# Kernel tuning notes

Hardware: AMD Instinct MI355X
Metric: run time of the kernel (lower is better)

## Reference

```python
import jax, jax.numpy as jnp
import numpy as np

L2_REG = 0.02


def setup_inputs() -> dict:
    key = jax.random.key(0)
    k1, k2 = jax.random.split(key)
    n, d = 4096, 1024
    anchors = jax.random.normal(k1, (n, d), dtype=jnp.float32)
    positives = jax.random.normal(k2, (n, d), dtype=jnp.float32)
    return {"anchors": anchors, "positives": positives}


def reference(anchors, positives):
    # Fused equivalent of the per-row masked_select loop:
    # x[i, j] = a_i . (p_j - p_i) = S[i, j] - S[i, i], for j != i
    n = anchors.shape[0]
    S = anchors @ positives.T                     # (n, n)
    x = S - jnp.diag(S)[:, None]                  # subtract anchor-positive sim per row
    offdiag = ~jnp.eye(n, dtype=bool)
    # sum over negatives j != i of exp(x[i, j])
    s = jnp.sum(jnp.where(offdiag, jnp.exp(x), 0.0), axis=1)  # (n,)
    n_pair = jnp.mean(jnp.log1p(s))
    l2 = jnp.sum(anchors ** 2 + positives ** 2) / n
    return n_pair + L2_REG * l2
```

## Files before the change

### kernel.cpp

```cpp
#include <hip/hip_runtime.h>
#include <math.h>
#include <stdint.h>

#define N 4096
#define Dm 1024
#define BK 64
#define NT (Dm / BK)
#define NCB (N / 64)
#define NPART 512

typedef __attribute__((ext_vector_type(8))) short bf16x8;
typedef __attribute__((ext_vector_type(4))) float f32x4;

typedef const void __attribute__((address_space(1)))* gas_t;
typedef void __attribute__((address_space(3)))* las_t;

static __device__ __forceinline__ void gload_lds16(const void* g, void* l) {
    __builtin_amdgcn_global_load_lds((gas_t)g, (las_t)l, 16, 0, 0);
}

static __device__ __forceinline__ unsigned short f2bf(float f) {
    unsigned int u = __float_as_uint(f);
    unsigned int r = (u + 0x7fff + ((u >> 16) & 1)) >> 16;
    return (unsigned short)r;
}

__global__ __launch_bounds__(256) void prep_kernel(const float* __restrict__ A,
                                                   const float* __restrict__ P,
                                                   unsigned short* __restrict__ Abf,
                                                   unsigned short* __restrict__ Pbf,
                                                   float* __restrict__ D,
                                                   float* __restrict__ rowl2,
                                                   float* __restrict__ accL,
                                                   float* __restrict__ accR,
                                                   unsigned int* __restrict__ ticket) {
    if (blockIdx.x == 0 && threadIdx.x == 0) {
        accL[0] = 0.0f; accR[0] = 0.0f; ticket[0] = 0u;
    }
    int t = threadIdx.x;
    int lane = t & 63;
    int row = blockIdx.x * 4 + (t >> 6);
    const float4* a4 = (const float4*)(A + (size_t)row * Dm);
    const float4* p4 = (const float4*)(P + (size_t)row * Dm);
    ushort4* ao = (ushort4*)(Abf + (size_t)row * Dm);
    ushort4* po = (ushort4*)(Pbf + (size_t)row * Dm);
    float dot = 0.0f, l2 = 0.0f;
#pragma unroll
    for (int c = 0; c < 4; ++c) {
        int idx = c * 64 + lane;
        float4 a = a4[idx], p = p4[idx];
        ushort4 ab, pb;
        ab.x = f2bf(a.x); ab.y = f2bf(a.y); ab.z = f2bf(a.z); ab.w = f2bf(a.w);
        pb.x = f2bf(p.x); pb.y = f2bf(p.y); pb.z = f2bf(p.z); pb.w = f2bf(p.w);
        ao[idx] = ab; po[idx] = pb;
        dot += a.x * p.x + a.y * p.y + a.z * p.z + a.w * p.w;
        l2  += a.x * a.x + a.y * a.y + a.z * a.z + a.w * a.w
             + p.x * p.x + p.y * p.y + p.z * p.z + p.w * p.w;
    }
#pragma unroll
    for (int off = 32; off; off >>= 1) {
        dot += __shfl_xor(dot, off, 64);
        l2  += __shfl_xor(l2,  off, 64);
    }
    if (lane == 0) {
        D[row]     = dot;
        rowl2[row] = l2;
    }
}

#define STAGE_TILE(gp, lp, kt) do {                                            \
        gload_lds16((gp) + (kt),                    (lp)         + tid * 8);   \
        gload_lds16((gp) + (kt) +  64 * (size_t)Dm, (lp) + 4096  + tid * 8);   \
        gload_lds16((gp) + (kt) + 128 * (size_t)Dm, (lp) + 8192  + tid * 8);   \
        gload_lds16((gp) + (kt) + 192 * (size_t)Dm, (lp) + 12288 + tid * 8);   \
    } while (0)

#define STAGE_B_HALF(lpB, kt, h) do {                                          \
        gload_lds16(gB + (kt) + ((h) ? 128 * (size_t)Dm : (size_t)0),          \
                    (lpB) + (h) * 8192 + tid * 8);                             \
        gload_lds16(gB + (kt) + ((h) ? 192 * (size_t)Dm : 64 * (size_t)Dm),    \
                    (lpB) + (h) * 8192 + 4096 + tid * 8);                      \
    } while (0)

#define READ_A4(dst, buf, rg0) do {                                            \
        dst[0] = *(const bf16x8*)((buf) + ((rg0)     * 16) * BK + aoff0);      \
        dst[1] = *(const bf16x8*)((buf) + ((rg0)     * 16) * BK + aoff1);      \
        dst[2] = *(const bf16x8*)((buf) + ((rg0) + 1) * 16 * BK + aoff0);      \
        dst[3] = *(const bf16x8*)((buf) + ((rg0) + 1) * 16 * BK + aoff1);      \
    } while (0)

#define READ_B8(buf) do {                                                      \
        _Pragma("unroll")                                                      \
        for (int j = 0; j < 4; ++j) {                                          \
            bfr[j][0] = *(const bf16x8*)((buf) + j * 16 * BK + aoff0);         \
            bfr[j][1] = *(const bf16x8*)((buf) + j * 16 * BK + aoff1);         \
        }                                                                      \
    } while (0)

#define MFMA_PH(P, ap)                                                         \
    _Pragma("unroll")                                                          \
    for (int j = 0; j < 4; ++j)                                                \
        acc[2*(P)][j]   = __builtin_amdgcn_mfma_f32_16x16x32_bf16(ap[0], bfr[j][0], acc[2*(P)][j],   0, 0, 0); \
    _Pragma("unroll")                                                          \
    for (int j = 0; j < 4; ++j)                                                \
        acc[2*(P)][j]   = __builtin_amdgcn_mfma_f32_16x16x32_bf16(ap[1], bfr[j][1], acc[2*(P)][j],   0, 0, 0); \
    _Pragma("unroll")                                                          \
    for (int j = 0; j < 4; ++j)                                                \
        acc[2*(P)+1][j] = __builtin_amdgcn_mfma_f32_16x16x32_bf16(ap[2], bfr[j][0], acc[2*(P)+1][j], 0, 0, 0); \
    _Pragma("unroll")                                                          \
    for (int j = 0; j < 4; ++j)                                                \
        acc[2*(P)+1][j] = __builtin_amdgcn_mfma_f32_16x16x32_bf16(ap[3], bfr[j][1], acc[2*(P)+1][j], 0, 0, 0);

#define MFMA_PH3_REFILL(ap, bufn, DOREFILL)                                    \
    _Pragma("unroll")                                                          \
    for (int j = 0; j < 4; ++j) {                                              \
        acc[6][j] = __builtin_amdgcn_mfma_f32_16x16x32_bf16(ap[0], bfr[j][0], acc[6][j], 0, 0, 0); \
        acc[6][j] = __builtin_amdgcn_mfma_f32_16x16x32_bf16(ap[1], bfr[j][1], acc[6][j], 0, 0, 0); \
        acc[7][j] = __builtin_amdgcn_mfma_f32_16x16x32_bf16(ap[2], bfr[j][0], acc[7][j], 0, 0, 0); \
        acc[7][j] = __builtin_amdgcn_mfma_f32_16x16x32_bf16(ap[3], bfr[j][1], acc[7][j], 0, 0, 0); \
        if (DOREFILL) {                                                        \
            bfr[j][0] = *(const bf16x8*)((bufn) + j * 16 * BK + aoff0);        \
            bfr[j][1] = *(const bf16x8*)((bufn) + j * 16 * BK + aoff1);        \
        }                                                                      \
    }

#define PHASE_EDGE() do {                                                      \
        __builtin_amdgcn_sched_barrier(0);                                     \
        __builtin_amdgcn_s_barrier();                                          \
        asm volatile("s_waitcnt lgkmcnt(0)" ::: "memory");                     \
        __builtin_amdgcn_sched_barrier(0);                                     \
    } while (0)

#define TILE_BODY(CUR, NXT) do {                                               \
        const unsigned short* aT  = aBase + (CUR) * 16384;                     \
        const unsigned short* aTn = aBase + (NXT) * 16384;                     \
        const unsigned short* bTn = bBase + (NXT) * 16384;                     \
        unsigned short* stA = &As[NXT][0];                                     \
        unsigned short* stB = &Bs[CUR][0];                                     \
           \
        READ_A4(aF[1], aT, 2);                                                 \
        if (t >= 1 && t <= 14) STAGE_TILE(gA, stA, (t + 1) * BK);              \
        __builtin_amdgcn_s_setprio(1);                                         \
        MFMA_PH(0, aF[0])                                                      \
        __builtin_amdgcn_s_setprio(0);                                         \
        PHASE_EDGE();                                                          \
             \
        READ_A4(aF[0], aT, 4);                                                 \
        if (t <= 13) STAGE_B_HALF(stB, (t + 2) * BK, 0);                       \
        __builtin_amdgcn_s_setprio(1);                                         \
        MFMA_PH(1, aF[1])                                                      \
        __builtin_amdgcn_s_setprio(0);                                         \
        PHASE_EDGE();                                                          \
             \
        READ_A4(aF[1], aT, 6);                                                 \
        if (t <= 13) STAGE_B_HALF(stB, (t + 2) * BK, 1);                       \
        __builtin_amdgcn_s_setprio(1);                                         \
        MFMA_PH(2, aF[0])                                                      \
        __builtin_amdgcn_s_setprio(0);                                         \
        PHASE_EDGE();                                                          \
        \
             \
        if (t <= 13)      { asm volatile("s_waitcnt vmcnt(4)" ::: "memory"); } \
        else if (t == 14) { asm volatile("s_waitcnt vmcnt(0)" ::: "memory"); } \
        if (t <= 14) __builtin_amdgcn_s_barrier();                             \
        __builtin_amdgcn_sched_barrier(0);                                     \
        __builtin_amdgcn_s_setprio(1);                                         \
        MFMA_PH3_REFILL(aF[1], bTn, (t <= 14))                                 \
        __builtin_amdgcn_s_setprio(0);                                         \
        if (t <= 14) {                                                         \
            READ_A4(aF[0], aTn, 0);                                            \
            PHASE_EDGE();                                                      \
        }                                                                      \
    } while (0)

__global__ __launch_bounds__(512, 2) void npair_mfma(const unsigned short* __restrict__ Abf,
                                                     const unsigned short* __restrict__ Pbf,
                                                     float* __restrict__ Mpart,
                                                     float* __restrict__ Spart) {
    __shared__ unsigned short As[2][256 * BK];
    __shared__ unsigned short Bs[2][256 * BK];

    int tid = threadIdx.x;
    int lane = tid & 63;
    int wid = tid >> 6;
    int wr = wid >> 2, wc = wid & 3;

    int bid = blockIdx.y * gridDim.x + blockIdx.x;
    int xcd = bid & 7, lid = bid >> 3;
    int by = (xcd >> 1) * 4 + (lid >> 3);
    int bx = (xcd & 1) * 8 + (lid & 7);
    int row0 = by * 256, col0 = bx * 256;

    int srow = tid >> 3;
    int kcol = (tid & 7) ^ (srow & 7);
    const unsigned short* gA = Abf + (size_t)(row0 + srow) * Dm + (kcol << 3);
    const unsigned short* gB = Pbf + (size_t)(col0 + srow) * Dm + (kcol << 3);

    STAGE_TILE(gA, &As[0][0], 0);
    STAGE_TILE(gB, &Bs[0][0], 0);
    STAGE_TILE(gA, &As[1][0], BK);
    STAGE_TILE(gB, &Bs[1][0], BK);
    asm volatile("s_waitcnt vmcnt(8)" ::: "memory");
    __builtin_amdgcn_s_barrier();

    int l15 = lane & 15;
    int aoff0 = (((lane >> 4)    ) ^ (lane & 7)) << 3;
    int aoff1 = (((lane >> 4) + 4) ^ (lane & 7)) << 3;
    const unsigned short* aBase = &As[0][0] + (wr * 128 + l15) * BK;
    const unsigned short* bBase = &Bs[0][0] + (wc * 64  + l15) * BK;

    f32x4 acc[8][4] = {};
    bf16x8 bfr[4][2];
    bf16x8 aF[2][4];

    READ_B8(bBase);
    READ_A4(aF[0], aBase, 0);
    __builtin_amdgcn_sched_barrier(0);
    asm volatile("s_waitcnt lgkmcnt(0)" ::: "memory");
    __builtin_amdgcn_sched_barrier(0);

    for (int tt = 0; tt < NT / 2; ++tt) {
        int t = 2 * tt;
        TILE_BODY(0, 1);
        t = 2 * tt + 1;
        TILE_BODY(1, 0);
    }

    __builtin_amdgcn_sched_barrier(0);

    int cb = bx * 4 + wc;
#pragma unroll
    for (int i = 0; i < 8; ++i) {
        int rloc = wr * 128 + i * 16 + ((lane >> 4) << 2);
#pragma unroll
        for (int e = 0; e < 4; ++e) {
            int gr = row0 + rloc + e;
            float xs[4];
            float m = -INFINITY;
#pragma unroll
            for (int j = 0; j < 4; ++j) {
                int gc = col0 + wc * 64 + j * 16 + (lane & 15);
                float x = acc[i][j][e];
                if (gr == gc) x = -INFINITY;
                xs[j] = x;
                m = fmaxf(m, x);
            }
#pragma unroll
            for (int off = 8; off; off >>= 1) m = fmaxf(m, __shfl_xor(m, off, 64));
            float s = 0.0f;
#pragma unroll
            for (int j = 0; j < 4; ++j) s += __expf(xs[j] - m);
#pragma unroll
            for (int off = 8; off; off >>= 1) s += __shfl_xor(s, off, 64);
            if ((lane & 15) == 0) {
                Mpart[(size_t)gr * NCB + cb] = m;
                Spart[(size_t)gr * NCB + cb] = s;
            }
        }
    }
}

__global__ __launch_bounds__(256) void combine_final(const float* __restrict__ Mpart,
                                                     const float* __restrict__ Spart,
                                                     const float* __restrict__ D,
                                                     const float* __restrict__ rowl2,
                                                     float* __restrict__ accL,
                                                     float* __restrict__ accR,
                                                     unsigned int* __restrict__ ticket,
                                                     float* __restrict__ out) {
    int t = threadIdx.x;
    int lane = t & 63;
    int w = t >> 6;
    __shared__ float ls[8];
#pragma unroll
    for (int r = 0; r < 2; ++r) {
        int row = blockIdx.x * 8 + w * 2 + r;
        float mp = Mpart[(size_t)row * NCB + lane];
        float sp = Spart[(size_t)row * NCB + lane];
        float m = mp;
#pragma unroll
        for (int off = 32; off; off >>= 1) m = fmaxf(m, __shfl_xor(m, off, 64));
        float s = sp * __expf(mp - m);
#pragma unroll
        for (int off = 32; off; off >>= 1) s += __shfl_xor(s, off, 64);
        if (lane == 0) {
            float z = m + logf(s) - D[row];
            ls[w * 2 + r] = fmaxf(z, 0.0f) + log1pf(__expf(-fabsf(z)));
        }
    }
    __syncthreads();
    if (t == 0) {
        int r8 = blockIdx.x * 8;
        float L = 0.0f, R = 0.0f;
#pragma unroll
        for (int r = 0; r < 8; ++r) { L += ls[r]; R += rowl2[r8 + r]; }
        atomicAdd(accL, L);
        atomicAdd(accR, R);
        __threadfence();
        unsigned int done = atomicAdd(ticket, 1u);
        if (done == NPART - 1) {
            float aL = atomicAdd(accL, 0.0f);
            float aR = atomicAdd(accR, 0.0f);
            out[0] = aL / (float)N + 0.02f * (aR / (float)N);
        }
    }
}

extern "C" void kernel_launch(void* const* d_in, const int* in_sizes, int n_in,
                              void* d_out, int out_size, void* d_ws, size_t ws_size,
                              hipStream_t stream) {
    const float* A = (const float*)d_in[0];
    const float* P = (const float*)d_in[1];
    float* out = (float*)d_out;

    unsigned short* Abf = (unsigned short*)d_ws;
    unsigned short* Pbf = Abf + (size_t)N * Dm;
    float* D     = (float*)(Pbf + (size_t)N * Dm);
    float* rowl2 = D + N;
    float* accL  = rowl2 + N;
    float* accR  = accL + 1;
    unsigned int* ticket = (unsigned int*)(accR + 1);
    float* Mpart = (float*)(ticket + 1);
    float* Spart = Mpart + (size_t)N * NCB;

    prep_kernel<<<N / 4, 256, 0, stream>>>(A, P, Abf, Pbf, D, rowl2, accL, accR, ticket);
    dim3 grid(16, 16);
    npair_mfma<<<grid, 512, 0, stream>>>(Abf, Pbf, Mpart, Spart);
    combine_final<<<N / 8, 256, 0, stream>>>(Mpart, Spart, D, rowl2, accL, accR, ticket, out);
}
```

Measured before the change: 134.7 us.

## Fuse prep, GEMM and combine into one cooperative kernel with grid syncs

Replaces the three launches (bf16 conversion/prep, MFMA GEMM with partial log-sum-exp, final combine) with a single cooperative kernel of 256 blocks, separated by grid-wide syncs. Each block now converts 16 rows, runs its GEMM tile, then combines 16 rows, and block 0 writes the final output after a last grid sync. This removes two kernel launch gaps and the ticket-based completion counter. In exchange it adds the cost of cooperative launch and grid barriers, and the prep phase runs with fewer, larger blocks than before.

```diff
diff --git a/kernel.cpp b/kernel.cpp
--- a/kernel.cpp
+++ b/kernel.cpp
@@ -1,13 +1,15 @@
 #include <hip/hip_runtime.h>
+#include <hip/hip_cooperative_groups.h>
 #include <math.h>
 #include <stdint.h>
+
+namespace cg = cooperative_groups;
 
 #define N 4096
 #define Dm 1024
 #define BK 64
 #define NT (Dm / BK)
 #define NCB (N / 64)
-#define NPART 512
 
 typedef __attribute__((ext_vector_type(8))) short bf16x8;
 typedef __attribute__((ext_vector_type(4))) float f32x4;
@@ -23,49 +25,6 @@
     unsigned int u = __float_as_uint(f);
     unsigned int r = (u + 0x7fff + ((u >> 16) & 1)) >> 16;
     return (unsigned short)r;
-}
-
-__global__ __launch_bounds__(256) void prep_kernel(const float* __restrict__ A,
-                                                   const float* __restrict__ P,
-                                                   unsigned short* __restrict__ Abf,
-                                                   unsigned short* __restrict__ Pbf,
-                                                   float* __restrict__ D,
-                                                   float* __restrict__ rowl2,
-                                                   float* __restrict__ accL,
-                                                   float* __restrict__ accR,
-                                                   unsigned int* __restrict__ ticket) {
-    if (blockIdx.x == 0 && threadIdx.x == 0) {
-        accL[0] = 0.0f; accR[0] = 0.0f; ticket[0] = 0u;
-    }
-    int t = threadIdx.x;
-    int lane = t & 63;
-    int row = blockIdx.x * 4 + (t >> 6);
-    const float4* a4 = (const float4*)(A + (size_t)row * Dm);
-    const float4* p4 = (const float4*)(P + (size_t)row * Dm);
-    ushort4* ao = (ushort4*)(Abf + (size_t)row * Dm);
-    ushort4* po = (ushort4*)(Pbf + (size_t)row * Dm);
-    float dot = 0.0f, l2 = 0.0f;
-#pragma unroll
-    for (int c = 0; c < 4; ++c) {
-        int idx = c * 64 + lane;
-        float4 a = a4[idx], p = p4[idx];
-        ushort4 ab, pb;
-        ab.x = f2bf(a.x); ab.y = f2bf(a.y); ab.z = f2bf(a.z); ab.w = f2bf(a.w);
-        pb.x = f2bf(p.x); pb.y = f2bf(p.y); pb.z = f2bf(p.z); pb.w = f2bf(p.w);
-        ao[idx] = ab; po[idx] = pb;
-        dot += a.x * p.x + a.y * p.y + a.z * p.z + a.w * p.w;
-        l2  += a.x * a.x + a.y * a.y + a.z * a.z + a.w * a.w
-             + p.x * p.x + p.y * p.y + p.z * p.z + p.w * p.w;
-    }
-#pragma unroll
-    for (int off = 32; off; off >>= 1) {
-        dot += __shfl_xor(dot, off, 64);
-        l2  += __shfl_xor(l2,  off, 64);
-    }
-    if (lane == 0) {
-        D[row]     = dot;
-        rowl2[row] = l2;
-    }
 }
 
 #define STAGE_TILE(gp, lp, kt) do {                                            \
@@ -137,29 +96,24 @@
         const unsigned short* bTn = bBase + (NXT) * 16384;                     \
         unsigned short* stA = &As[NXT][0];                                     \
         unsigned short* stB = &Bs[CUR][0];                                     \
-           \
         READ_A4(aF[1], aT, 2);                                                 \
         if (t >= 1 && t <= 14) STAGE_TILE(gA, stA, (t + 1) * BK);              \
         __builtin_amdgcn_s_setprio(1);                                         \
         MFMA_PH(0, aF[0])                                                      \
         __builtin_amdgcn_s_setprio(0);                                         \
         PHASE_EDGE();                                                          \
-             \
         READ_A4(aF[0], aT, 4);                                                 \
         if (t <= 13) STAGE_B_HALF(stB, (t + 2) * BK, 0);                       \
         __builtin_amdgcn_s_setprio(1);                                         \
         MFMA_PH(1, aF[1])                                                      \
         __builtin_amdgcn_s_setprio(0);                                         \
         PHASE_EDGE();                                                          \
-             \
         READ_A4(aF[1], aT, 6);                                                 \
         if (t <= 13) STAGE_B_HALF(stB, (t + 2) * BK, 1);                       \
         __builtin_amdgcn_s_setprio(1);                                         \
         MFMA_PH(2, aF[0])                                                      \
         __builtin_amdgcn_s_setprio(0);                                         \
         PHASE_EDGE();                                                          \
-        \
-             \
         if (t <= 13)      { asm volatile("s_waitcnt vmcnt(4)" ::: "memory"); } \
         else if (t == 14) { asm volatile("s_waitcnt vmcnt(0)" ::: "memory"); } \
         if (t <= 14) __builtin_amdgcn_s_barrier();                             \
@@ -173,19 +127,63 @@
         }                                                                      \
     } while (0)
 
-__global__ __launch_bounds__(512, 2) void npair_mfma(const unsigned short* __restrict__ Abf,
-                                                     const unsigned short* __restrict__ Pbf,
-                                                     float* __restrict__ Mpart,
-                                                     float* __restrict__ Spart) {
+__global__ __launch_bounds__(512, 2) void fused_npair(const float* __restrict__ A,
+                                                      const float* __restrict__ P,
+                                                      unsigned short* __restrict__ Abf,
+                                                      unsigned short* __restrict__ Pbf,
+                                                      float* __restrict__ D,
+                                                      float* __restrict__ rowl2,
+                                                      float* __restrict__ accL,
+                                                      float* __restrict__ accR,
+                                                      float* __restrict__ Mpart,
+                                                      float* __restrict__ Spart,
+                                                      float* __restrict__ out) {
     __shared__ unsigned short As[2][256 * BK];
     __shared__ unsigned short Bs[2][256 * BK];
+
+    cg::grid_group grid = cg::this_grid();
 
     int tid = threadIdx.x;
     int lane = tid & 63;
     int wid = tid >> 6;
+    int bid = blockIdx.x;
+
+    if (bid == 0 && tid == 0) { accL[0] = 0.0f; accR[0] = 0.0f; }
+#pragma unroll
+    for (int r = 0; r < 2; ++r) {
+        int row = bid * 16 + wid * 2 + r;
+        const float4* a4 = (const float4*)(A + (size_t)row * Dm);
+        const float4* p4 = (const float4*)(P + (size_t)row * Dm);
+        ushort4* ao = (ushort4*)(Abf + (size_t)row * Dm);
+        ushort4* po = (ushort4*)(Pbf + (size_t)row * Dm);
+        float dot = 0.0f, l2 = 0.0f;
+#pragma unroll
+        for (int c = 0; c < 4; ++c) {
+            int idx = c * 64 + lane;
+            float4 a = a4[idx], p = p4[idx];
+            ushort4 ab, pb;
+            ab.x = f2bf(a.x); ab.y = f2bf(a.y); ab.z = f2bf(a.z); ab.w = f2bf(a.w);
+            pb.x = f2bf(p.x); pb.y = f2bf(p.y); pb.z = f2bf(p.z); pb.w = f2bf(p.w);
+            ao[idx] = ab; po[idx] = pb;
+            dot += a.x * p.x + a.y * p.y + a.z * p.z + a.w * p.w;
+            l2  += a.x * a.x + a.y * a.y + a.z * a.z + a.w * a.w
+                 + p.x * p.x + p.y * p.y + p.z * p.z + p.w * p.w;
+        }
+#pragma unroll
+        for (int off = 32; off; off >>= 1) {
+            dot += __shfl_xor(dot, off, 64);
+            l2  += __shfl_xor(l2,  off, 64);
+        }
+        if (lane == 0) { D[row] = dot; rowl2[row] = l2; }
+    }
+    __threadfence();
+    grid.sync();
+
+    asm volatile("s_waitcnt vmcnt(0) lgkmcnt(0)" ::: "memory");
+    __builtin_amdgcn_sched_barrier(0);
+
     int wr = wid >> 2, wc = wid & 3;
 
-    int bid = blockIdx.y * gridDim.x + blockIdx.x;
     int xcd = bid & 7, lid = bid >> 3;
     int by = (xcd >> 1) * 4 + (lid >> 3);
     int bx = (xcd & 1) * 8 + (lid & 7);
@@ -225,7 +223,6 @@
         t = 2 * tt + 1;
         TILE_BODY(1, 0);
     }
-
     __builtin_amdgcn_sched_barrier(0);
 
     int cb = bx * 4 + wc;
@@ -258,23 +255,13 @@
             }
         }
     }
-}
-
-__global__ __launch_bounds__(256) void combine_final(const float* __restrict__ Mpart,
-                                                     const float* __restrict__ Spart,
-                                                     const float* __restrict__ D,
-                                                     const float* __restrict__ rowl2,
-                                                     float* __restrict__ accL,
-                                                     float* __restrict__ accR,
-                                                     unsigned int* __restrict__ ticket,
-                                                     float* __restrict__ out) {
-    int t = threadIdx.x;
-    int lane = t & 63;
-    int w = t >> 6;
-    __shared__ float ls[8];
+    __threadfence();
+    grid.sync();
+
+    float* ls = (float*)&As[0][0];
 #pragma unroll
     for (int r = 0; r < 2; ++r) {
-        int row = blockIdx.x * 8 + w * 2 + r;
+        int row = bid * 16 + wid * 2 + r;
         float mp = Mpart[(size_t)row * NCB + lane];
         float sp = Spart[(size_t)row * NCB + lane];
         float m = mp;
@@ -285,24 +272,24 @@
         for (int off = 32; off; off >>= 1) s += __shfl_xor(s, off, 64);
         if (lane == 0) {
             float z = m + logf(s) - D[row];
-            ls[w * 2 + r] = fmaxf(z, 0.0f) + log1pf(__expf(-fabsf(z)));
+            ls[wid * 2 + r] = fmaxf(z, 0.0f) + log1pf(__expf(-fabsf(z)));
         }
     }
     __syncthreads();
-    if (t == 0) {
-        int r8 = blockIdx.x * 8;
+    if (tid == 0) {
         float L = 0.0f, R = 0.0f;
 #pragma unroll
-        for (int r = 0; r < 8; ++r) { L += ls[r]; R += rowl2[r8 + r]; }
+        for (int r = 0; r < 16; ++r) { L += ls[r]; R += rowl2[bid * 16 + r]; }
         atomicAdd(accL, L);
         atomicAdd(accR, R);
-        __threadfence();
-        unsigned int done = atomicAdd(ticket, 1u);
-        if (done == NPART - 1) {
-            float aL = atomicAdd(accL, 0.0f);
-            float aR = atomicAdd(accR, 0.0f);
-            out[0] = aL / (float)N + 0.02f * (aR / (float)N);
-        }
+    }
+    __threadfence();
+    grid.sync();
+
+    if (bid == 0 && tid == 0) {
+        float aL = atomicAdd(accL, 0.0f);
+        float aR = atomicAdd(accR, 0.0f);
+        out[0] = aL / (float)N + 0.02f * (aR / (float)N);
     }
 }
 
@@ -319,12 +306,12 @@
     float* rowl2 = D + N;
     float* accL  = rowl2 + N;
     float* accR  = accL + 1;
-    unsigned int* ticket = (unsigned int*)(accR + 1);
-    float* Mpart = (float*)(ticket + 1);
+    float* Mpart = accR + 1;
     float* Spart = Mpart + (size_t)N * NCB;
 
-    prep_kernel<<<N / 4, 256, 0, stream>>>(A, P, Abf, Pbf, D, rowl2, accL, accR, ticket);
-    dim3 grid(16, 16);
-    npair_mfma<<<grid, 512, 0, stream>>>(Abf, Pbf, Mpart, Spart);
-    combine_final<<<N / 8, 256, 0, stream>>>(Mpart, Spart, D, rowl2, accL, accR, ticket, out);
+    void* args[] = { (void*)&A, (void*)&P, (void*)&Abf, (void*)&Pbf,
+                     (void*)&D, (void*)&rowl2, (void*)&accL, (void*)&accR,
+                     (void*)&Mpart, (void*)&Spart, (void*)&out };
+    hipLaunchCooperativeKernel((void*)fused_npair, dim3(256), dim3(512),
+                               args, 0, stream);
 }
```

Result: slower. 356.5 us (+164.6%).
